# Optimization experiments

Measured on AMD Instinct MI355X. Metric: run time of the kernel, lower is better.

Reference implementation:

```python
import jax, jax.numpy as jnp
import numpy as np

D_MODEL = 768
N_HEADS = 12
D_K = D_MODEL // N_HEADS


def setup_inputs() -> dict:
    key = jax.random.key(0)
    kq, kk, kv, kwq, kbq, kwo, kbo = jax.random.split(key, 7)
    B, S = 1, 4096
    s = 1.0 / np.sqrt(D_MODEL)
    return {
        "q": jax.random.normal(kq, (B, S, D_MODEL), jnp.float32),
        "k": jax.random.normal(kk, (B, S, D_MODEL), jnp.float32),
        "v": jax.random.normal(kv, (B, S, D_MODEL), jnp.float32),
        # nn.Linear weights stored as [out, in]; note the original forward
        # uses W_q for Q, K, AND V (W_k/W_v are never used), so only W_q and
        # W_o are materialized here.
        "Wq": jax.random.uniform(kwq, (D_MODEL, D_MODEL), jnp.float32, -s, s),
        "bq": jax.random.uniform(kbq, (D_MODEL,), jnp.float32, -s, s),
        "Wo": jax.random.uniform(kwo, (D_MODEL, D_MODEL), jnp.float32, -s, s),
        "bo": jax.random.uniform(kbo, (D_MODEL,), jnp.float32, -s, s),
    }


def _split_heads(x):  # [B,S,D] -> [B,H,S,Dk]
    B, S, _ = x.shape
    return x.reshape(B, S, N_HEADS, D_K).transpose(0, 2, 1, 3)


def reference(q, k, v, Wq, bq, Wo, bo):
    # Faithful to source: same W_q projection applied to q, k, v.
    Q = _split_heads(q @ Wq.T + bq)
    K = _split_heads(k @ Wq.T + bq)
    V = _split_heads(v @ Wq.T + bq)
    scale = 1.0 / np.sqrt(D_K).astype(np.float32)
    scores = jnp.einsum("bhqd,bhkd->bhqk", Q, K) * scale  # [B,H,S,S]
    probs = jax.nn.softmax(scores, axis=-1)
    atten = jnp.einsum("bhqk,bhkd->bhqd", probs, V)
    B, _, S, _ = atten.shape
    concat = atten.transpose(0, 2, 1, 3).reshape(B, S, D_MODEL)
    return concat @ Wo.T + bo
```

## Files before the change

kernel.cpp:

```cpp
#include <hip/hip_runtime.h>
#include <stdint.h>
#include <math.h>


#define SQ 4096
#define DM 768
#define NH 12

typedef float f32x4 __attribute__((ext_vector_type(4)));
typedef short bf16x8 __attribute__((ext_vector_type(8)));
typedef unsigned int u32x4 __attribute__((ext_vector_type(4)));
typedef unsigned short ushort_t;

static __device__ __forceinline__ ushort_t f2bf(float f) {
    unsigned int u = __builtin_bit_cast(unsigned int, f);
    u += 0x7fffu + ((u >> 16) & 1u);
    return (ushort_t)(u >> 16);
}

static __device__ __forceinline__ unsigned int cvt_pk_bf16(float a, float b) {
    unsigned int d;
    asm("v_cvt_pk_bf16_f32 %0, %1, %2" : "=v"(d) : "v"(a), "v"(b));
    return d;
}

static __device__ __forceinline__ float exp2_hw(float x) {
    float r;
    asm("v_exp_f32 %0, %1" : "=v"(r) : "v"(x));
    return r;
}

static __device__ __forceinline__ void gload16(const ushort_t* g, ushort_t* l) {
    __builtin_amdgcn_global_load_lds(
        reinterpret_cast<const __attribute__((address_space(1))) unsigned int*>(
            reinterpret_cast<uintptr_t>(g)),
        reinterpret_cast<__attribute__((address_space(3))) unsigned int*>(
            reinterpret_cast<uintptr_t>(l)),
        16, 0, 0);
}

__global__ __launch_bounds__(256) void cvt_all(
    const float* __restrict__ q, const float* __restrict__ k,
    const float* __restrict__ v, const float* __restrict__ Wq,
    const float* __restrict__ Wo, ushort_t* __restrict__ xb,
    ushort_t* __restrict__ wqb, ushort_t* __restrict__ wob) {
    const int NE4 = (SQ * DM) / 4;
    const int NW4 = (DM * DM) / 4;
    int i = blockIdx.x * 256 + threadIdx.x;
    const float* src;
    ushort_t* dst;
    if (i < NE4) { src = q; dst = xb; }
    else if (i < 2 * NE4) { src = k; dst = xb + SQ * DM; i -= NE4; }
    else if (i < 3 * NE4) { src = v; dst = xb + 2 * SQ * DM; i -= 2 * NE4; }
    else if (i < 3 * NE4 + NW4) { src = Wq; dst = wqb; i -= 3 * NE4; }
    else if (i < 3 * NE4 + 2 * NW4) { src = Wo; dst = wob; i -= 3 * NE4 + NW4; }
    else return;
    float4 x = reinterpret_cast<const float4*>(src)[i];
    ushort4 o;
    o.x = f2bf(x.x); o.y = f2bf(x.y); o.z = f2bf(x.z); o.w = f2bf(x.w);
    reinterpret_cast<ushort4*>(dst)[i] = o;
}

template <int EPI>
__global__ __launch_bounds__(256) void gemm_bf16(
    const ushort_t* __restrict__ A, const ushort_t* __restrict__ B,
    const float* __restrict__ bias, ushort_t* __restrict__ proj,
    ushort_t* __restrict__ vt, float* __restrict__ outf) {
    __shared__ __align__(16) ushort_t lsA[128 * 64];
    __shared__ __align__(16) ushort_t lsB[128 * 64];
    const int tid = threadIdx.x;
    const int lane = tid & 63;
    const int w = tid >> 6;
    const int wm = w >> 1, wn = w & 1;
    const int g = lane >> 4, li = lane & 15;
    const int NB = (EPI == 2) ? 32 : 6;
    const int bm = blockIdx.x / NB, bn = blockIdx.x % NB;
    const int arow = bm * 128, brow = bn * 128;
    const int sr = lane >> 3;
    const int sc = ((lane & 7) ^ sr) * 8;

    f32x4 acc[4][4] = {};

    for (int kt = 0; kt < 12; ++kt) {
        const int k0 = kt * 64;
        __syncthreads();
#pragma unroll
        for (int c = 0; c < 4; ++c) {
            const int chunk = w * 4 + c;
            const int r = chunk * 8 + sr;
            gload16(A + (size_t)(arow + r) * DM + k0 + sc, lsA + chunk * 512);
            gload16(B + (size_t)(brow + r) * DM + k0 + sc, lsB + chunk * 512);
        }
        __syncthreads();

        bf16x8 af[4][2];
#pragma unroll
        for (int mf = 0; mf < 4; ++mf) {
            const int row = wm * 64 + mf * 16 + li;
#pragma unroll
            for (int ks = 0; ks < 2; ++ks)
                af[mf][ks] = *reinterpret_cast<const bf16x8*>(
                    lsA + row * 64 + ((ks * 32 + g * 8) ^ ((li & 7) << 3)));
        }
#pragma unroll
        for (int nf = 0; nf < 4; ++nf) {
            const int row = wn * 64 + nf * 16 + li;
            bf16x8 b0 = *reinterpret_cast<const bf16x8*>(
                lsB + row * 64 + ((g * 8) ^ ((li & 7) << 3)));
            bf16x8 b1 = *reinterpret_cast<const bf16x8*>(
                lsB + row * 64 + ((32 + g * 8) ^ ((li & 7) << 3)));
#pragma unroll
            for (int mf = 0; mf < 4; ++mf) {
                acc[mf][nf] = __builtin_amdgcn_mfma_f32_16x16x32_bf16(af[mf][0], b0, acc[mf][nf], 0, 0, 0);
                acc[mf][nf] = __builtin_amdgcn_mfma_f32_16x16x32_bf16(af[mf][1], b1, acc[mf][nf], 0, 0, 0);
            }
        }
    }

    if (EPI == 0) {
        const float qscale = (arow < 4096) ? 0.18033688011112042f : 1.0f;
#pragma unroll
        for (int nf = 0; nf < 4; ++nf) {
            const int col = brow + wn * 64 + nf * 16 + li;
            const float bv = bias[col];
#pragma unroll
            for (int mf = 0; mf < 4; ++mf) {
                const int row0 = arow + wm * 64 + mf * 16 + g * 4;
#pragma unroll
                for (int r = 0; r < 4; ++r)
                    proj[(size_t)(row0 + r) * DM + col] = f2bf((acc[mf][nf][r] + bv) * qscale);
            }
        }
    } else if (EPI == 2) {
        float bv[4][4];
#pragma unroll
        for (int mf = 0; mf < 4; ++mf)
#pragma unroll
            for (int r = 0; r < 4; ++r)
                bv[mf][r] = bias[arow + wm * 64 + mf * 16 + g * 4 + r];
#pragma unroll
        for (int nf = 0; nf < 4; ++nf) {
            const int j = brow + wn * 64 + nf * 16 + li;
            const int pos = (j & ~31) | ((j & 0xC) << 1) | (((j >> 4) & 1) << 2) | (j & 3);
#pragma unroll
            for (int mf = 0; mf < 4; ++mf) {
                const int row0 = arow + wm * 64 + mf * 16 + g * 4;
#pragma unroll
                for (int r = 0; r < 4; ++r)
                    vt[(size_t)(row0 + r) * SQ + pos] = f2bf(acc[mf][nf][r] + bv[mf][r]);
            }
        }
    } else {
#pragma unroll
        for (int nf = 0; nf < 4; ++nf) {
            const int col = brow + wn * 64 + nf * 16 + li;
            const float bv = bias[col];
#pragma unroll
            for (int mf = 0; mf < 4; ++mf) {
                const int row0 = arow + wm * 64 + mf * 16 + g * 4;
#pragma unroll
                for (int r = 0; r < 4; ++r)
                    outf[(size_t)(row0 + r) * DM + col] = acc[mf][nf][r] + bv;
            }
        }
    }
}

__global__ __launch_bounds__(256) void attn_bf16(
    const ushort_t* __restrict__ qk, const ushort_t* __restrict__ vtb,
    ushort_t* __restrict__ cc) {
    __shared__ __align__(16) ushort_t kl[2][2][32 * 64];
    __shared__ __align__(16) ushort_t vl[2][2][64 * 32];

    const int tid = threadIdx.x, lane = tid & 63, w = tid >> 6;
    const int wp = w & 1, p = w >> 1;
    const int g = lane >> 4, li = lane & 15;
    const int logical = (blockIdx.x & 7) * 96 + (blockIdx.x >> 3);
    const int h = logical >> 6, qb = logical & 63;
    const int sr = lane >> 3;
    const int sc = ((lane & 7) ^ sr) * 8;
    const int vdr = lane >> 2;
    const int vsc = ((lane & 3) ^ ((lane >> 3) & 3)) * 8;

    const ushort_t* Kb = qk + (size_t)(4096 + p * 2048) * DM + (size_t)h * 64;
    const ushort_t* Vb = vtb + (size_t)(h * 64) * SQ + p * 2048;

    bf16x8 qf[2][2];
#pragma unroll
    for (int qh = 0; qh < 2; ++qh)
#pragma unroll
        for (int ks = 0; ks < 2; ++ks)
            qf[qh][ks] = *reinterpret_cast<const bf16x8*>(
                qk + (size_t)(qb * 64 + wp * 32 + qh * 16 + li) * DM + h * 64 + ks * 32 + g * 8);

    f32x4 oacc[2][4] = {};
    float lsum0 = 0.f, lsum1 = 0.f;

#pragma unroll
    for (int c = 0; c < 2; ++c) {
        const int ch = wp * 2 + c;
        gload16(Kb + (size_t)(ch * 8 + sr) * DM + sc, &kl[p][0][ch * 512]);
        gload16(Vb + (size_t)(ch * 16 + vdr) * SQ + vsc, &vl[p][0][ch * 512]);
    }
    __syncthreads();

#define STEP(kp, vp, kn, vn, kvn)                                              \
    do {                                                                       \
        if ((kvn) < 64) {                                                      \
            const int kvo = (kvn) * 32;                                        \
            _Pragma("unroll") for (int c = 0; c < 2; ++c) {                    \
                const int ch = wp * 2 + c;                                     \
                gload16(Kb + (size_t)(kvo + ch * 8 + sr) * DM + sc,            \
                        &(kn)[ch * 512]);                                      \
                gload16(Vb + (size_t)(ch * 16 + vdr) * SQ + kvo + vsc,         \
                        &(vn)[ch * 512]);                                      \
            }                                                                  \
        }                                                                      \
        f32x4 sf[2][2] = {};                                                   \
        __builtin_amdgcn_s_setprio(1);                                         \
        _Pragma("unroll") for (int nf = 0; nf < 2; ++nf) {                     \
            const int row = nf * 16 + li;                                      \
            bf16x8 kb0 = *reinterpret_cast<const bf16x8*>(                     \
                (kp) + row * 64 + ((g * 8) ^ ((li & 7) << 3)));                \
            bf16x8 kb1 = *reinterpret_cast<const bf16x8*>(                     \
                (kp) + row * 64 + ((32 + g * 8) ^ ((li & 7) << 3)));           \
            _Pragma("unroll") for (int qh = 0; qh < 2; ++qh) {                 \
                sf[qh][nf] = __builtin_amdgcn_mfma_f32_16x16x32_bf16(          \
                    kb0, qf[qh][0], sf[qh][nf], 0, 0, 0);                      \
                sf[qh][nf] = __builtin_amdgcn_mfma_f32_16x16x32_bf16(          \
                    kb1, qf[qh][1], sf[qh][nf], 0, 0, 0);                      \
            }                                                                  \
        }                                                                      \
        __builtin_amdgcn_s_setprio(0);                                         \
        _Pragma("unroll") for (int qh = 0; qh < 2; ++qh)                       \
            _Pragma("unroll") for (int nf = 0; nf < 2; ++nf) {                 \
                f32x4 pe;                                                      \
                _Pragma("unroll") for (int r = 0; r < 4; ++r)                  \
                    pe[r] = exp2_hw(sf[qh][nf][r]);                            \
                sf[qh][nf] = pe;                                               \
                const float ps = (pe[0] + pe[1]) + (pe[2] + pe[3]);            \
                if (qh == 0) lsum0 += ps; else lsum1 += ps;                    \
            }                                                                  \
        __builtin_amdgcn_s_setprio(1);                                         \
        bf16x8 pa[2];                                                          \
        _Pragma("unroll") for (int qh = 0; qh < 2; ++qh) {                     \
            u32x4 pu;                                                          \
            pu.x = cvt_pk_bf16(sf[qh][0][0], sf[qh][0][1]);                    \
            pu.y = cvt_pk_bf16(sf[qh][0][2], sf[qh][0][3]);                    \
            pu.z = cvt_pk_bf16(sf[qh][1][0], sf[qh][1][1]);                    \
            pu.w = cvt_pk_bf16(sf[qh][1][2], sf[qh][1][3]);                    \
            pa[qh] = __builtin_bit_cast(bf16x8, pu);                           \
        }                                                                      \
        _Pragma("unroll") for (int nv = 0; nv < 4; ++nv) {                     \
            const int vrow = nv * 16 + li;                                     \
            bf16x8 vb = *reinterpret_cast<const bf16x8*>(                      \
                (vp) + vrow * 32 + ((g ^ ((li >> 1) & 3)) * 8));               \
            oacc[0][nv] = __builtin_amdgcn_mfma_f32_16x16x32_bf16(             \
                pa[0], vb, oacc[0][nv], 0, 0, 0);                              \
            oacc[1][nv] = __builtin_amdgcn_mfma_f32_16x16x32_bf16(             \
                pa[1], vb, oacc[1][nv], 0, 0, 0);                              \
        }                                                                      \
        __builtin_amdgcn_s_setprio(0);                                         \
        __syncthreads();                                                       \
    } while (0)

    {
        ushort_t* k0p = &kl[p][0][0];
        ushort_t* v0p = &vl[p][0][0];
        ushort_t* k1p = &kl[p][1][0];
        ushort_t* v1p = &vl[p][1][0];
#pragma unroll 1
        for (int t = 0; t < 32; ++t) {
            STEP(k0p, v0p, k1p, v1p, 2 * t + 1);
            STEP(k1p, v1p, k0p, v0p, 2 * t + 2);
        }
    }
#undef STEP

    float* ob = reinterpret_cast<float*>(&kl[0][0][0]);
    float* lsb = ob + 4096;
    if (p == 1) {
#pragma unroll
        for (int qh = 0; qh < 2; ++qh) {
#pragma unroll
            for (int nv = 0; nv < 4; ++nv)
                *reinterpret_cast<f32x4*>(
                    ob + (((wp * 2 + qh) * 4 + nv) * 64 + lane) * 4) = oacc[qh][nv];
            lsb[(wp * 2 + qh) * 64 + lane] = (qh == 0) ? lsum0 : lsum1;
        }
    }
    __syncthreads();
    if (p == 0) {
        lsum0 += lsb[(wp * 2 + 0) * 64 + lane];
        lsum1 += lsb[(wp * 2 + 1) * 64 + lane];
#pragma unroll
        for (int qh = 0; qh < 2; ++qh)
#pragma unroll
            for (int nv = 0; nv < 4; ++nv) {
                f32x4 o = *reinterpret_cast<const f32x4*>(
                    ob + (((wp * 2 + qh) * 4 + nv) * 64 + lane) * 4);
                oacc[qh][nv] += o;
            }

#pragma unroll
        for (int qh = 0; qh < 2; ++qh) {
            float s = (qh == 0) ? lsum0 : lsum1;
            s += __shfl_xor(s, 16);
            s += __shfl_xor(s, 32);
            float inv[4];
            const int gbase = g << 2;
#pragma unroll
            for (int r = 0; r < 4; ++r)
                inv[r] = 1.0f / __shfl(s, gbase + r);
#pragma unroll
            for (int nv = 0; nv < 4; ++nv)
#pragma unroll
                for (int r = 0; r < 4; ++r) {
                    const int row = qb * 64 + wp * 32 + qh * 16 + g * 4 + r;
                    const int col = h * 64 + nv * 16 + li;
                    cc[(size_t)row * DM + col] = f2bf(oacc[qh][nv][r] * inv[r]);
                }
        }
    }
}

extern "C" void kernel_launch(void* const* d_in, const int* in_sizes, int n_in,
                              void* d_out, int out_size, void* d_ws, size_t ws_size,
                              hipStream_t stream) {
    const float* q = (const float*)d_in[0];
    const float* k = (const float*)d_in[1];
    const float* v = (const float*)d_in[2];
    const float* Wq = (const float*)d_in[3];
    const float* bq = (const float*)d_in[4];
    const float* Wo = (const float*)d_in[5];
    const float* bo = (const float*)d_in[6];
    float* out = (float*)d_out;

    ushort_t* ws = (ushort_t*)d_ws;
    const int NE = SQ * DM;
    ushort_t* xb = ws;
    ushort_t* wqb = ws + 3 * NE;
    ushort_t* wob = wqb + DM * DM;
    ushort_t* proj = wob + DM * DM;
    ushort_t* vt = proj + 2 * NE;
    ushort_t* cc = vt + NE;

    const int n4 = 3 * (NE / 4) + 2 * ((DM * DM) / 4);
    cvt_all<<<(n4 + 255) / 256, 256, 0, stream>>>(q, k, v, Wq, Wo, xb, wqb, wob);

    gemm_bf16<0><<<(8192 / 128) * 6, 256, 0, stream>>>(xb, wqb, bq, proj, (ushort_t*)nullptr, (float*)nullptr);

    gemm_bf16<2><<<(768 / 128) * 32, 256, 0, stream>>>(wqb, xb + 2 * NE, bq, (ushort_t*)nullptr, vt, (float*)nullptr);

    attn_bf16<<<NH * (SQ / 64), 256, 0, stream>>>(proj, vt, cc);

    gemm_bf16<1><<<(SQ / 128) * 6, 256, 0, stream>>>(cc, wob, bo, (ushort_t*)nullptr, (ushort_t*)nullptr, out);
}
```

Baseline: 137.5 us.

## Split KV across four independent waves with private LDS buffers and MFMA row sums

The attention kernel changes from two wave-pairs sharing KV tiles to four waves, each owning a quarter of the KV sequence and all 64 query rows. Each wave stages into private LDS double buffers and orders them with vmcnt waits instead of per-step block barriers. Softmax row sums now come from an extra MFMA against a ones vector rather than scalar adds and shuffles. This trades higher register pressure (20 accumulators, 8 query fragments) and a larger 64KB LDS footprint, which may cut occupancy, for fewer barriers and a cheaper denominator.

After: 156.5 us. 13.8% more time.

```diff
diff --git a/kernel.cpp b/kernel.cpp
--- a/kernel.cpp
+++ b/kernel.cpp
@@ -38,6 +38,11 @@
             reinterpret_cast<uintptr_t>(l)),
         16, 0, 0);
 }
+
+#define WAITV8 do { asm volatile("s_waitcnt vmcnt(8)" ::: "memory"); \
+                    __builtin_amdgcn_sched_barrier(0); } while (0)
+#define WAITV0 do { asm volatile("s_waitcnt vmcnt(0)" ::: "memory"); \
+                    __builtin_amdgcn_sched_barrier(0); } while (0)
 
 __global__ __launch_bounds__(256) void cvt_all(
     const float* __restrict__ q, const float* __restrict__ k,
@@ -169,11 +174,9 @@
 __global__ __launch_bounds__(256) void attn_bf16(
     const ushort_t* __restrict__ qk, const ushort_t* __restrict__ vtb,
     ushort_t* __restrict__ cc) {
-    __shared__ __align__(16) ushort_t kl[2][2][32 * 64];
-    __shared__ __align__(16) ushort_t vl[2][2][64 * 32];
+    __shared__ __align__(16) ushort_t smem[32768];
 
     const int tid = threadIdx.x, lane = tid & 63, w = tid >> 6;
-    const int wp = w & 1, p = w >> 1;
     const int g = lane >> 4, li = lane & 15;
     const int logical = (blockIdx.x & 7) * 96 + (blockIdx.x >> 3);
     const int h = logical >> 6, qb = logical & 63;
@@ -182,41 +185,54 @@
     const int vdr = lane >> 2;
     const int vsc = ((lane & 3) ^ ((lane >> 3) & 3)) * 8;
 
-    const ushort_t* Kb = qk + (size_t)(4096 + p * 2048) * DM + (size_t)h * 64;
-    const ushort_t* Vb = vtb + (size_t)(h * 64) * SQ + p * 2048;
-
-    bf16x8 qf[2][2];
-#pragma unroll
-    for (int qh = 0; qh < 2; ++qh)
+    const ushort_t* Kb = qk + (size_t)(4096 + w * 1024) * DM + (size_t)h * 64;
+    const ushort_t* Vb = vtb + (size_t)(h * 64) * SQ + w * 1024;
+
+    ushort_t* K0 = smem + w * 8192;
+    ushort_t* V0 = K0 + 2048;
+    ushort_t* K1 = K0 + 4096;
+    ushort_t* V1 = K0 + 6144;
+
+    bf16x8 qf[4][2];
+#pragma unroll
+    for (int qh = 0; qh < 4; ++qh)
 #pragma unroll
         for (int ks = 0; ks < 2; ++ks)
             qf[qh][ks] = *reinterpret_cast<const bf16x8*>(
-                qk + (size_t)(qb * 64 + wp * 32 + qh * 16 + li) * DM + h * 64 + ks * 32 + g * 8);
-
-    f32x4 oacc[2][4] = {};
-    float lsum0 = 0.f, lsum1 = 0.f;
-
-#pragma unroll
-    for (int c = 0; c < 2; ++c) {
-        const int ch = wp * 2 + c;
-        gload16(Kb + (size_t)(ch * 8 + sr) * DM + sc, &kl[p][0][ch * 512]);
-        gload16(Vb + (size_t)(ch * 16 + vdr) * SQ + vsc, &vl[p][0][ch * 512]);
-    }
-    __syncthreads();
-
-#define STEP(kp, vp, kn, vn, kvn)                                              \
+                qk + (size_t)(qb * 64 + qh * 16 + li) * DM + h * 64 + ks * 32 + g * 8);
+
+    f32x4 oacc[4][5] = {};
+
+    const unsigned int one2 = 0x3F803F80u;
+    u32x4 onesu = {one2, one2, one2, one2};
+    const bf16x8 vones = __builtin_bit_cast(bf16x8, onesu);
+
+    WAITV0;
+
+#pragma unroll
+    for (int c = 0; c < 4; ++c) {
+        gload16(Kb + (size_t)(c * 8 + sr) * DM + sc, K0 + c * 512);
+        gload16(Vb + (size_t)(c * 16 + vdr) * SQ + vsc, V0 + c * 512);
+    }
+
+#define STEP(kp, vp, kn, vn, nxt, DOSTAGE)                                     \
     do {                                                                       \
-        if ((kvn) < 64) {                                                      \
-            const int kvo = (kvn) * 32;                                        \
-            _Pragma("unroll") for (int c = 0; c < 2; ++c) {                    \
-                const int ch = wp * 2 + c;                                     \
-                gload16(Kb + (size_t)(kvo + ch * 8 + sr) * DM + sc,            \
-                        &(kn)[ch * 512]);                                      \
-                gload16(Vb + (size_t)(ch * 16 + vdr) * SQ + kvo + vsc,         \
-                        &(vn)[ch * 512]);                                      \
+        if (DOSTAGE) {                                                         \
+            const int kvo = (nxt) * 32;                                        \
+            _Pragma("unroll") for (int c = 0; c < 4; ++c) {                    \
+                gload16(Kb + (size_t)(kvo + c * 8 + sr) * DM + sc,             \
+                        (kn) + c * 512);                                       \
+                gload16(Vb + (size_t)(c * 16 + vdr) * SQ + kvo + vsc,          \
+                        (vn) + c * 512);                                       \
             }                                                                  \
+            WAITV8;                                                            \
+        } else {                                                               \
+            WAITV0;                                                            \
         }                                                                      \
-        f32x4 sf[2][2] = {};                                                   \
+        f32x4 sf[4][2];                                                        \
+        _Pragma("unroll") for (int qh = 0; qh < 4; ++qh)                       \
+            _Pragma("unroll") for (int nf = 0; nf < 2; ++nf)                   \
+                sf[qh][nf] = (f32x4){0.f, 0.f, 0.f, 0.f};                      \
         __builtin_amdgcn_s_setprio(1);                                         \
         _Pragma("unroll") for (int nf = 0; nf < 2; ++nf) {                     \
             const int row = nf * 16 + li;                                      \
@@ -224,7 +240,7 @@
                 (kp) + row * 64 + ((g * 8) ^ ((li & 7) << 3)));                \
             bf16x8 kb1 = *reinterpret_cast<const bf16x8*>(                     \
                 (kp) + row * 64 + ((32 + g * 8) ^ ((li & 7) << 3)));           \
-            _Pragma("unroll") for (int qh = 0; qh < 2; ++qh) {                 \
+            _Pragma("unroll") for (int qh = 0; qh < 4; ++qh) {                 \
                 sf[qh][nf] = __builtin_amdgcn_mfma_f32_16x16x32_bf16(          \
                     kb0, qf[qh][0], sf[qh][nf], 0, 0, 0);                      \
                 sf[qh][nf] = __builtin_amdgcn_mfma_f32_16x16x32_bf16(          \
@@ -232,91 +248,77 @@
             }                                                                  \
         }                                                                      \
         __builtin_amdgcn_s_setprio(0);                                         \
-        _Pragma("unroll") for (int qh = 0; qh < 2; ++qh)                       \
-            _Pragma("unroll") for (int nf = 0; nf < 2; ++nf) {                 \
-                f32x4 pe;                                                      \
-                _Pragma("unroll") for (int r = 0; r < 4; ++r)                  \
-                    pe[r] = exp2_hw(sf[qh][nf][r]);                            \
-                sf[qh][nf] = pe;                                               \
-                const float ps = (pe[0] + pe[1]) + (pe[2] + pe[3]);            \
-                if (qh == 0) lsum0 += ps; else lsum1 += ps;                    \
+        bf16x8 pa[4];                                                          \
+        _Pragma("unroll") for (int qh = 0; qh < 4; ++qh) {                     \
+            f32x4 p0, p1;                                                      \
+            _Pragma("unroll") for (int r = 0; r < 4; ++r) {                    \
+                p0[r] = exp2_hw(sf[qh][0][r]);                                 \
+                p1[r] = exp2_hw(sf[qh][1][r]);                                 \
             }                                                                  \
-        __builtin_amdgcn_s_setprio(1);                                         \
-        bf16x8 pa[2];                                                          \
-        _Pragma("unroll") for (int qh = 0; qh < 2; ++qh) {                     \
             u32x4 pu;                                                          \
-            pu.x = cvt_pk_bf16(sf[qh][0][0], sf[qh][0][1]);                    \
-            pu.y = cvt_pk_bf16(sf[qh][0][2], sf[qh][0][3]);                    \
-            pu.z = cvt_pk_bf16(sf[qh][1][0], sf[qh][1][1]);                    \
-            pu.w = cvt_pk_bf16(sf[qh][1][2], sf[qh][1][3]);                    \
+            pu.x = cvt_pk_bf16(p0[0], p0[1]);                                  \
+            pu.y = cvt_pk_bf16(p0[2], p0[3]);                                  \
+            pu.z = cvt_pk_bf16(p1[0], p1[1]);                                  \
+            pu.w = cvt_pk_bf16(p1[2], p1[3]);                                  \
             pa[qh] = __builtin_bit_cast(bf16x8, pu);                           \
         }                                                                      \
+        __builtin_amdgcn_s_setprio(1);                                         \
         _Pragma("unroll") for (int nv = 0; nv < 4; ++nv) {                     \
             const int vrow = nv * 16 + li;                                     \
             bf16x8 vb = *reinterpret_cast<const bf16x8*>(                      \
                 (vp) + vrow * 32 + ((g ^ ((li >> 1) & 3)) * 8));               \
-            oacc[0][nv] = __builtin_amdgcn_mfma_f32_16x16x32_bf16(             \
-                pa[0], vb, oacc[0][nv], 0, 0, 0);                              \
-            oacc[1][nv] = __builtin_amdgcn_mfma_f32_16x16x32_bf16(             \
-                pa[1], vb, oacc[1][nv], 0, 0, 0);                              \
+            _Pragma("unroll") for (int qh = 0; qh < 4; ++qh)                   \
+                oacc[qh][nv] = __builtin_amdgcn_mfma_f32_16x16x32_bf16(        \
+                    pa[qh], vb, oacc[qh][nv], 0, 0, 0);                        \
         }                                                                      \
+        _Pragma("unroll") for (int qh = 0; qh < 4; ++qh)                       \
+            oacc[qh][4] = __builtin_amdgcn_mfma_f32_16x16x32_bf16(             \
+                pa[qh], vones, oacc[qh][4], 0, 0, 0);                          \
         __builtin_amdgcn_s_setprio(0);                                         \
-        __syncthreads();                                                       \
     } while (0)
 
-    {
-        ushort_t* k0p = &kl[p][0][0];
-        ushort_t* v0p = &vl[p][0][0];
-        ushort_t* k1p = &kl[p][1][0];
-        ushort_t* v1p = &vl[p][1][0];
 #pragma unroll 1
-        for (int t = 0; t < 32; ++t) {
-            STEP(k0p, v0p, k1p, v1p, 2 * t + 1);
-            STEP(k1p, v1p, k0p, v0p, 2 * t + 2);
-        }
-    }
+    for (int t = 0; t < 15; ++t) {
+        STEP(K0, V0, K1, V1, 2 * t + 1, true);
+        STEP(K1, V1, K0, V0, 2 * t + 2, true);
+    }
+    STEP(K0, V0, K1, V1, 31, true);
+    STEP(K1, V1, K0, V0, 32, false);
 #undef STEP
 
-    float* ob = reinterpret_cast<float*>(&kl[0][0][0]);
-    float* lsb = ob + 4096;
-    if (p == 1) {
-#pragma unroll
-        for (int qh = 0; qh < 2; ++qh) {
+    __syncthreads();
+    float* ob = reinterpret_cast<float*>(smem);
+    if (w > 0) {
+        float* base = ob + (w - 1) * 5120;
+#pragma unroll
+        for (int qh = 0; qh < 4; ++qh)
+#pragma unroll
+            for (int nv = 0; nv < 5; ++nv)
+                *reinterpret_cast<f32x4*>(
+                    base + ((qh * 5 + nv) * 64 + lane) * 4) = oacc[qh][nv];
+    }
+    __syncthreads();
+    if (w == 0) {
+#pragma unroll
+        for (int j = 0; j < 3; ++j) {
+            const float* base = ob + j * 5120;
+#pragma unroll
+            for (int qh = 0; qh < 4; ++qh)
+#pragma unroll
+                for (int nv = 0; nv < 5; ++nv)
+                    oacc[qh][nv] += *reinterpret_cast<const f32x4*>(
+                        base + ((qh * 5 + nv) * 64 + lane) * 4);
+        }
+#pragma unroll
+        for (int qh = 0; qh < 4; ++qh) {
+            float inv[4];
+#pragma unroll
+            for (int r = 0; r < 4; ++r) inv[r] = 1.0f / oacc[qh][4][r];
 #pragma unroll
             for (int nv = 0; nv < 4; ++nv)
-                *reinterpret_cast<f32x4*>(
-                    ob + (((wp * 2 + qh) * 4 + nv) * 64 + lane) * 4) = oacc[qh][nv];
-            lsb[(wp * 2 + qh) * 64 + lane] = (qh == 0) ? lsum0 : lsum1;
-        }
-    }
-    __syncthreads();
-    if (p == 0) {
-        lsum0 += lsb[(wp * 2 + 0) * 64 + lane];
-        lsum1 += lsb[(wp * 2 + 1) * 64 + lane];
-#pragma unroll
-        for (int qh = 0; qh < 2; ++qh)
-#pragma unroll
-            for (int nv = 0; nv < 4; ++nv) {
-                f32x4 o = *reinterpret_cast<const f32x4*>(
-                    ob + (((wp * 2 + qh) * 4 + nv) * 64 + lane) * 4);
-                oacc[qh][nv] += o;
-            }
-
-#pragma unroll
-        for (int qh = 0; qh < 2; ++qh) {
-            float s = (qh == 0) ? lsum0 : lsum1;
-            s += __shfl_xor(s, 16);
-            s += __shfl_xor(s, 32);
-            float inv[4];
-            const int gbase = g << 2;
-#pragma unroll
-            for (int r = 0; r < 4; ++r)
-                inv[r] = 1.0f / __shfl(s, gbase + r);
-#pragma unroll
-            for (int nv = 0; nv < 4; ++nv)
 #pragma unroll
                 for (int r = 0; r < 4; ++r) {
-                    const int row = qb * 64 + wp * 32 + qh * 16 + g * 4 + r;
+                    const int row = qb * 64 + qh * 16 + g * 4 + r;
                     const int col = h * 64 + nv * 16 + li;
                     cc[(size_t)row * DM + col] = f2bf(oacc[qh][nv][r] * inv[r]);
                 }
```
